# Optimization experiments

Measured on AMD Instinct MI355X. Metric: run time of the kernel, lower is better.

The kernel has to match this reference:

```python
import jax, jax.numpy as jnp
import numpy as np

B, T_ENC, T_DEC, E = 16, 512, 128, 512
H = 1024


def setup_inputs() -> dict:
    key = jax.random.key(0)
    ks = jax.random.split(key, 16)
    def rn(k, shape, s=0.02):
        return jax.random.normal(k, shape, jnp.float32) * s
    z = lambda *s: jnp.zeros(s, jnp.float32)
    return {
        "inputs": jax.random.normal(ks[0], (B, T_ENC, E), jnp.float32),
        "padded_mels": jax.random.normal(ks[1], (B, 80, T_DEC), jnp.float32),
        "W_enc": rn(ks[2], (128, E)),
        "W_q": rn(ks[3], (128, H)),
        "W_loc_conv": rn(ks[4], (32, 1, 31)),
        "b_loc_conv": z(32),
        "W_loc_dense": rn(ks[5], (128, 32)),
        "b_loc_dense": z(128),
        "w_e": rn(ks[6], (1, 128)),
        "b_e": z(1),
        "W_p1": rn(ks[7], (256, 80)),
        "W_p2": rn(ks[8], (256, 256)),
        "W_ih1": rn(ks[9], (4 * H, 256 + E)),
        "W_hh1": rn(ks[10], (4 * H, H)),
        "b_ih1": z(4 * H),
        "b_hh1": z(4 * H),
        "W_ih2": rn(ks[11], (4 * H, H)),
        "W_hh2": rn(ks[12], (4 * H, H)),
        "b_ih2": z(4 * H),
        "b_hh2": z(4 * H),
        "W_proj": rn(ks[13], (80, H + E)),
        "b_proj": z(80),
        "W_stop": rn(ks[14], (1, H + E)),
        "b_stop": z(1),
    }


def _lstm_cell(x, h, c, W_ih, W_hh, b_ih, b_hh):
    g = W_ih @ x + b_ih + W_hh @ h + b_hh
    i, f, gg, o = jnp.split(g, 4)  # torch gate order: i, f, g, o
    c = jax.nn.sigmoid(f) * c + jax.nn.sigmoid(i) * jnp.tanh(gg)
    h = jax.nn.sigmoid(o) * jnp.tanh(c)
    return h, c


def _forward(inputs, padded_mels, W_enc, W_q, W_loc_conv, b_loc_conv,
             W_loc_dense, b_loc_dense, w_e, b_e, W_p1, W_p2,
             W_ih1, W_hh1, b_ih1, b_hh1, W_ih2, W_hh2, b_ih2, b_hh2,
             W_proj, b_proj, W_stop, b_stop):
    proc_enc = inputs @ W_enc.T  # (B, T_enc, 128)
    # prepend zero frame, use frames 0..T_dec-1 as teacher-forced inputs
    prev = jnp.concatenate([jnp.zeros((B, 80, 1), inputs.dtype), padded_mels], axis=-1)[:, :, :T_DEC]
    prev = jnp.transpose(prev, (2, 0, 1))  # (T_dec, B, 80)
    # F.dropout(p=0.5) in source defaults to training=True -> always applied; deterministic masks here
    mk = jax.random.key(42)
    m1 = jax.random.bernoulli(jax.random.fold_in(mk, 0), 0.5, (T_DEC, B, 256)).astype(inputs.dtype) * 2.0
    m2 = jax.random.bernoulli(jax.random.fold_in(mk, 1), 0.5, (T_DEC, B, 256)).astype(inputs.dtype) * 2.0

    def lstm2(x_seq):
        # faithful to source: (B,1,768) fed to batch_first=False nn.LSTM ->
        # sequence runs over the batch dim with batch=1 and zero init state each step
        zv = jnp.zeros((H,), x_seq.dtype)
        def cell(carry, x):
            h1, c1, h2, c2 = carry
            h1, c1 = _lstm_cell(x, h1, c1, W_ih1, W_hh1, b_ih1, b_hh1)
            h2, c2 = _lstm_cell(h1, h2, c2, W_ih2, W_hh2, b_ih2, b_hh2)
            return (h1, c1, h2, c2), h2
        _, hs = jax.lax.scan(cell, (zv, zv, zv, zv), x_seq)
        return hs  # (B, 1024)

    def step(carry, xs):
        cum, ctx = carry  # (B, T_enc), (B, E)
        x, d1, d2 = xs
        p = jax.nn.relu(x @ W_p1.T) * d1
        p = jax.nn.relu(p @ W_p2.T) * d2
        h = lstm2(jnp.concatenate([p, ctx], axis=-1))  # (B, 1024)
        q = h @ W_q.T  # (B, 128)
        loc = jax.lax.conv_general_dilated(
            cum[:, None, :], W_loc_conv, (1,), [(15, 15)],
            dimension_numbers=("NCH", "OIH", "NCH")) + b_loc_conv[None, :, None]  # (B, 32, T_enc)
        loc = jnp.transpose(loc, (0, 2, 1)) @ W_loc_dense.T + b_loc_dense  # (B, T_enc, 128)
        e = jnp.tanh(q[:, None, :] + loc + proc_enc) @ w_e[0] + b_e[0]  # (B, T_enc)
        aw = jax.nn.softmax(e, axis=1)
        new_ctx = jnp.einsum("bt,bte->be", aw, inputs)  # (B, E)
        do = jnp.concatenate([h, new_ctx], axis=-1)  # (B, 1536)
        frame = do @ W_proj.T + b_proj  # (B, 80)
        stop = do @ W_stop[0] + b_stop[0]  # (B,)
        return (cum + aw, new_ctx), (frame, stop)

    carry0 = (jnp.zeros((B, T_ENC), inputs.dtype), jnp.zeros((B, E), inputs.dtype))
    _, (mels, stops) = jax.lax.scan(step, carry0, (prev, m1, m2))
    return jnp.transpose(mels, (1, 0, 2)), jnp.transpose(stops, (1, 0))


def reference(inputs, padded_mels, W_enc, W_q, W_loc_conv, b_loc_conv,
              W_loc_dense, b_loc_dense, w_e, b_e, W_p1, W_p2,
              W_ih1, W_hh1, b_ih1, b_hh1, W_ih2, W_hh2, b_ih2, b_hh2,
              W_proj, b_proj, W_stop, b_stop):
    return _forward(inputs, padded_mels, W_enc, W_q, W_loc_conv, b_loc_conv,
                    W_loc_dense, b_loc_dense, w_e, b_e, W_p1, W_p2,
                    W_ih1, W_hh1, b_ih1, b_hh1, W_ih2, W_hh2, b_ih2, b_hh2,
                    W_proj, b_proj, W_stop, b_stop)
```

## Files before the change

### kernel.cpp

```cpp
#include <hip/hip_runtime.h>
#include <hip/hip_bf16.h>
#include <stdint.h>

#define TD 128
#define NB 16
#define TE 512
#define EE 512
#define HH 1024
#define NM 80
#define PP 256
#define NWG 256
#define NTH 512

#define AGENT __HIP_MEMORY_SCOPE_AGENT

typedef float f32x4 __attribute__((ext_vector_type(4)));

__device__ inline void astoref(float* p, float v) {
  __hip_atomic_store(p, v, __ATOMIC_RELAXED, AGENT);
}
__device__ inline void astored(double* p, double v) {
  __hip_atomic_store(p, v, __ATOMIC_RELAXED, AGENT);
}
__device__ inline f32x4 ntload4(const float* p) {
  f32x4 r;
  asm volatile("global_load_dwordx4 %0, %1, off sc0\n\ts_waitcnt vmcnt(0)"
               : "=&v"(r) : "v"(p) : "memory");
  return r;
}
__device__ inline float ntload1f(const float* p) {
  float r;
  asm volatile("global_load_dword %0, %1, off sc0\n\ts_waitcnt vmcnt(0)"
               : "=&v"(r) : "v"(p) : "memory");
  return r;
}
__device__ inline double ntload1d(const double* p) {
  double r;
  asm volatile("global_load_dwordx2 %0, %1, off sc0\n\ts_waitcnt vmcnt(0)"
               : "=&v"(r) : "v"(p) : "memory");
  return r;
}
__device__ inline double dsig(double x) { return 1.0 / (1.0 + exp(-x)); }

__host__ __device__ inline void threefry2x32(uint32_t k0, uint32_t k1,
                                             uint32_t& x0, uint32_t& x1) {
  uint32_t ks0 = k0, ks1 = k1, ks2 = k0 ^ k1 ^ 0x1BD11BDAu;
  x0 += ks0; x1 += ks1;
#define RND(rot) { x0 += x1; x1 = (x1 << (rot)) | (x1 >> (32 - (rot))); x1 ^= x0; }
  RND(13) RND(15) RND(26) RND(6)
  x0 += ks1; x1 += ks2 + 1u;
  RND(17) RND(29) RND(16) RND(24)
  x0 += ks2; x1 += ks0 + 2u;
  RND(13) RND(15) RND(26) RND(6)
  x0 += ks0; x1 += ks1 + 3u;
  RND(17) RND(29) RND(16) RND(24)
  x0 += ks1; x1 += ks2 + 4u;
  RND(13) RND(15) RND(26) RND(6)
  x0 += ks2; x1 += ks0 + 5u;
#undef RND
}

__device__ inline double mask_val(uint32_t ka, uint32_t kb, uint32_t i) {
  uint32_t x0 = 0u, x1 = i;
  threefry2x32(ka, kb, x0, x1);
  uint32_t bits = x0 ^ x1;
  float u = __uint_as_float((bits >> 9) | 0x3f800000u) - 1.0f;
  return (u < 0.5f) ? 2.0 : 0.0;
}

__global__ void k_proc_enc(const float* __restrict__ inputs,
                           const float* __restrict__ W_enc,
                           float* __restrict__ procTf) {
  int blk = blockIdx.x;
  int b = blk >> 5;
  int t0 = (blk & 31) * 16;
  int d = threadIdx.x;
  __shared__ float in_l[16][EE];
  for (int idx = threadIdx.x; idx < 16 * EE; idx += blockDim.x) {
    int tt = idx >> 9, e = idx & 511;
    in_l[tt][e] = inputs[((size_t)(b * TE + t0 + tt)) * EE + e];
  }
  __syncthreads();
  double acc[16];
#pragma unroll
  for (int tt = 0; tt < 16; ++tt) acc[tt] = 0.0;
  const float* wr = W_enc + (size_t)d * EE;
  for (int e = 0; e < EE; ++e) {
    double w = (double)wr[e];
#pragma unroll
    for (int tt = 0; tt < 16; ++tt) acc[tt] += w * (double)in_l[tt][e];
  }
  for (int tt = 0; tt < 16; ++tt)
    procTf[((size_t)(b * 128 + d)) * TE + t0 + tt] = (float)acc[tt];
}

__global__ void k_p(const float* __restrict__ pm, const float* __restrict__ Wp1,
                    const float* __restrict__ Wp2,
                    uint32_t k1a, uint32_t k1b, uint32_t k2a, uint32_t k2b,
                    float* __restrict__ p_allf) {
  int sb = blockIdx.x;
  int s = sb >> 4, b = sb & 15;
  int tid = threadIdx.x;
  uint32_t mi = (uint32_t)(sb * PP + tid);
  double d1 = mask_val(k1a, k1b, mi);
  double d2 = mask_val(k2a, k2b, mi);
  __shared__ float x_l[NM];
  __shared__ double p1_l[PP];
  if (tid < NM) x_l[tid] = (s == 0) ? 0.f : pm[(b * NM + tid) * TD + (s - 1)];
  __syncthreads();
  double a = 0.0;
  const float* w1 = Wp1 + tid * NM;
  for (int m = 0; m < NM; ++m) a += (double)w1[m] * (double)x_l[m];
  a = fmax(a, 0.0) * d1;
  p1_l[tid] = a;
  __syncthreads();
  double c = 0.0;
  const float* w2 = Wp2 + tid * PP;
  for (int k = 0; k < PP; ++k) c += (double)w2[k] * p1_l[k];
  c = fmax(c, 0.0) * d2;
  p_allf[sb * PP + tid] = (float)c;
}

__global__ void k_init(double* __restrict__ cumg, float* __restrict__ ctxf,
                       float* __restrict__ h1f, float* __restrict__ h2f,
                       uint32_t* __restrict__ barmem) {
  int tid = threadIdx.x;
  for (int i = tid; i < NB * TE; i += 256) cumg[i] = 0.0;
  for (int i = tid; i < NB * EE; i += 256) ctxf[i] = 0.f;
  for (int i = tid; i < 2 * HH; i += 256) { h1f[i] = 0.f; h2f[i] = 0.f; }
  for (int i = tid; i < 8192; i += 256) barmem[i] = 0u;
}

struct SMEM {
  float wldT[4096];
  float wcl[992];
  double bld[128], we[128], blc[32];
  double b1l[16], b2l[16];
  double g1l[16][16];
  double gA[16], gBC[16];
  double c1l[4], c2l[4];
  double be0;
  union U {
    struct { float h1[1024], h2[1024]; } cell;
    struct { float h[1024]; } pq;
    struct { float ctxall[8192]; } g1p;
    struct { double cum[64], q[128], loc[32][33]; } att;
    struct { float aw[512]; double red[16][32]; } ctxp;
    struct { double red[16]; } soft;
    struct { float hb[1536]; double red[16]; } outp;
  } u;
};

__device__ inline void gridbar(uint32_t* barmem, uint32_t& lgen, int wg, int tid) {
  __syncthreads();
  lgen++;
  if (wg == 0) {
    if (tid == 0)
      (void)__hip_atomic_load(&barmem[0], __ATOMIC_ACQUIRE, AGENT);
    if (tid >= 256 && tid < 511) {
      const uint32_t* fl = &barmem[(tid - 255) * 16];
      while (__hip_atomic_load(fl, __ATOMIC_RELAXED, AGENT) < lgen)
        __builtin_amdgcn_s_sleep(1);
    }
    __syncthreads();
    if (tid < 256) {
      asm volatile("s_waitcnt vmcnt(0)" ::: "memory");
      __hip_atomic_store(&barmem[4096 + tid * 16], lgen, __ATOMIC_RELAXED, AGENT);
    }
  } else {
    if (tid == 0) {
      (void)__hip_atomic_load(&barmem[wg * 16], __ATOMIC_ACQUIRE, AGENT);
      __hip_atomic_store(&barmem[wg * 16], lgen, __ATOMIC_RELAXED, AGENT);
      while (__hip_atomic_load(&barmem[4096 + wg * 16], __ATOMIC_RELAXED, AGENT) < lgen)
        __builtin_amdgcn_s_sleep(1);
    }
  }
  __syncthreads();
}

__global__ __launch_bounds__(NTH)
__attribute__((amdgpu_waves_per_eu(2, 2)))
void k_persist(
    const float* __restrict__ inputs,
    const float* __restrict__ W_q,
    const float* __restrict__ W_lc, const float* __restrict__ b_lc,
    const float* __restrict__ W_ld, const float* __restrict__ b_ld,
    const float* __restrict__ w_e, const float* __restrict__ b_e,
    const float* __restrict__ W_ih1, const float* __restrict__ W_hh1,
    const float* __restrict__ b_ih1, const float* __restrict__ b_hh1,
    const float* __restrict__ W_ih2, const float* __restrict__ W_hh2,
    const float* __restrict__ b_ih2, const float* __restrict__ b_hh2,
    const float* __restrict__ W_proj, const float* __restrict__ b_proj,
    const float* __restrict__ W_stop, const float* __restrict__ b_stop,
    const float* __restrict__ p_allf, const float* __restrict__ procTf,
    float* h1f, float* h2f, float* h_allf, float* qf,
    float* ef, float* awf, double* cumg, float* ctxf,
    uint32_t* barmem, float* out) {
  __shared__ SMEM sm;
  const int wg = blockIdx.x, tid = threadIdx.x;
  const int q = tid >> 5, l = tid & 31;
  const int row = (q >> 2) * 1024 + wg * 4 + (q & 3);
  uint32_t lgen = 0;

  for (int i = tid; i < 4096; i += NTH) sm.wldT[(i & 31) * 128 + (i >> 5)] = W_ld[i];
  for (int i = tid; i < 992; i += NTH) sm.wcl[i] = W_lc[i];
  for (int i = tid; i < 128; i += NTH) { sm.bld[i] = (double)b_ld[i]; sm.we[i] = (double)w_e[i]; }
  if (tid < 32) sm.blc[tid] = (double)b_lc[tid];
  if (tid == 0) sm.be0 = (double)b_e[0];
  if (l == 0) {
    sm.b1l[q] = (double)b_ih1[row] + (double)b_hh1[row];
    sm.b2l[q] = (double)b_ih2[row] + (double)b_hh2[row];
  }

  float wA[32], wB[32], wC[32], wD[24];
#pragma unroll
  for (int k = 0; k < 32; ++k) {
    int c = l + 32 * k;
    wA[k] = W_hh1[(size_t)row * 1024 + c];
    wB[k] = W_ih2[(size_t)row * 1024 + c];
    wC[k] = W_hh2[(size_t)row * 1024 + c];
  }
#pragma unroll
  for (int k = 0; k < 24; ++k) wD[k] = W_ih1[(size_t)row * 768 + l + 32 * k];
#pragma unroll
  for (int k = 0; k < 32; ++k) {
    asm volatile("" : "+v"(wA[k]));
    asm volatile("" : "+v"(wB[k]));
    asm volatile("" : "+v"(wC[k]));
  }
#pragma unroll
  for (int k = 0; k < 24; ++k) asm volatile("" : "+v"(wD[k]));
  __syncthreads();

  {
    for (int j = 0; j < 4; ++j) {
      f32x4 v = ntload4(ctxf + (tid + j * NTH) * 4);
      *(f32x4*)&sm.u.g1p.ctxall[(tid + j * NTH) * 4] = v;
    }
    __syncthreads();
    for (int b = 0; b < 16; ++b) {
      double a = 0.0;
#pragma unroll
      for (int k = 0; k < 8; ++k)
        a += (double)wD[k] * (double)p_allf[((size_t)0 * 16 + b) * 256 + l + 32 * k];
#pragma unroll
      for (int k = 8; k < 24; ++k)
        a += (double)wD[k] * (double)sm.u.g1p.ctxall[b * 512 + l + 32 * k - 256];
#pragma unroll
      for (int m = 1; m <= 16; m <<= 1) a += __shfl_xor(a, m);
      if (l == 0) sm.g1l[b][q] = a + sm.b1l[q];
    }
    __syncthreads();
  }
  gridbar(barmem, lgen, wg, tid);

  for (int s = 0; s < TD; ++s) {
    for (int r = 0; r <= 16; ++r) {
      if (r == 0 && tid < 4) { sm.c1l[tid] = 0.0; sm.c2l[tid] = 0.0; }
      if (tid < 256) {
        f32x4 v = ntload4(h1f + (((r & 1) ^ 1)) * 1024 + tid * 4);
        *(f32x4*)&sm.u.cell.h1[tid * 4] = v;
      } else if (r > 0) {
        f32x4 v = ntload4(h2f + (r & 1) * 1024 + (tid - 256) * 4);
        *(f32x4*)&sm.u.cell.h2[(tid - 256) * 4] = v;
      }
      __syncthreads();

      double a0 = 0.0, a1 = 0.0, a2 = 0.0;
#pragma unroll
      for (int k = 0; k < 32; ++k) {
        double h1v = (double)sm.u.cell.h1[l + 32 * k];
        a0 += (double)wA[k] * h1v;
        a1 += (double)wB[k] * h1v;
        a2 += (double)wC[k] * (double)sm.u.cell.h2[l + 32 * k];
      }
#pragma unroll
      for (int m = 1; m <= 16; m <<= 1) {
        a0 += __shfl_xor(a0, m);
        a1 += __shfl_xor(a1, m);
        a2 += __shfl_xor(a2, m);
      }
      if (l == 0) { sm.gA[q] = a0; sm.gBC[q] = a1 + a2; }
      __syncthreads();

      if (r < 16 && tid < 4) {
        int jj = tid;
        double gi = sm.g1l[r][jj]      + sm.gA[jj];
        double gf = sm.g1l[r][4 + jj]  + sm.gA[4 + jj];
        double gg = sm.g1l[r][8 + jj]  + sm.gA[8 + jj];
        double go = sm.g1l[r][12 + jj] + sm.gA[12 + jj];
        double cn = dsig(gf) * sm.c1l[jj] + dsig(gi) * tanh(gg);
        double hn = dsig(go) * tanh(cn);
        sm.c1l[jj] = cn;
        astoref(h1f + (r & 1) * 1024 + wg * 4 + jj, (float)hn);
      }
      if (r > 0 && tid >= 8 && tid < 12) {
        int jj = tid - 8, b = r - 1;
        double gi = sm.gBC[jj]      + sm.b2l[jj];
        double gf = sm.gBC[4 + jj]  + sm.b2l[4 + jj];
        double gg = sm.gBC[8 + jj]  + sm.b2l[8 + jj];
        double go = sm.gBC[12 + jj] + sm.b2l[12 + jj];
        double cn = dsig(gf) * sm.c2l[jj] + dsig(gi) * tanh(gg);
        double hn = dsig(go) * tanh(cn);
        sm.c2l[jj] = cn;
        astoref(h2f + ((b & 1)) * 1024 + wg * 4 + jj, (float)hn);
        astoref(h_allf + (size_t)b * 1024 + wg * 4 + jj, (float)hn);
      }
      gridbar(barmem, lgen, wg, tid);
    }

    {
      int b = wg >> 4;
      if (tid < 256) {
        f32x4 v = ntload4(h_allf + (size_t)b * 1024 + tid * 4);
        *(f32x4*)&sm.u.pq.h[tid * 4] = v;
      }
      __syncthreads();
      int o = tid >> 6, lane = tid & 63;
      int d = (wg & 15) * 8 + o;
      double a = 0.0;
#pragma unroll
      for (int k = 0; k < 16; ++k) {
        int c = lane + 64 * k;
        a += (double)W_q[(size_t)d * 1024 + c] * (double)sm.u.pq.h[c];
      }
#pragma unroll
      for (int m = 1; m <= 32; m <<= 1) a += __shfl_xor(a, m);
      if (lane == 0) astoref(qf + b * 128 + d, (float)a);
    }
    gridbar(barmem, lgen, wg, tid);

    {
      int b = wg >> 4, t0 = (wg & 15) * 32;
      if (tid < 62) {
        int g = t0 - 15 + tid;
        sm.u.att.cum[tid] = (g >= 0 && g < TE) ? ntload1d(cumg + b * TE + g) : 0.0;
      } else if (tid < 190) {
        sm.u.att.q[tid - 62] = (double)ntload1f(qf + b * 128 + (tid - 62));
      }
      __syncthreads();
#pragma unroll
      for (int it = 0; it < 2; ++it) {
        int task = tid + it * NTH;
        int t = task >> 5, ch = task & 31;
        double v = sm.blc[ch];
#pragma unroll
        for (int k = 0; k < 31; ++k) v += (double)sm.wcl[ch * 31 + k] * sm.u.att.cum[t + k];
        sm.u.att.loc[t][ch] = v;
      }
      __syncthreads();
      int t = tid >> 4, part = tid & 15;
      double en = 0.0;
      for (int k = 0; k < 8; ++k) {
        int d = part + 16 * k;
        double sv = sm.u.att.q[d] + sm.bld[d] +
                    (double)procTf[((size_t)(b * 128 + d)) * TE + t0 + t];
#pragma unroll
        for (int c = 0; c < 32; ++c)
          sv += sm.u.att.loc[t][c] * (double)sm.wldT[c * 128 + d];
        en += tanh(sv) * sm.we[d];
      }
#pragma unroll
      for (int m = 1; m <= 8; m <<= 1) en += __shfl_xor(en, m);
      if (part == 0) astoref(ef + b * TE + t0 + t, (float)(en + sm.be0));
    }
    gridbar(barmem, lgen, wg, tid);

    if (wg < 16) {
      int b = wg;
      double e = (double)ntload1f(ef + b * TE + tid);
      double mx = e;
#pragma unroll
      for (int m = 1; m <= 32; m <<= 1) mx = fmax(mx, __shfl_xor(mx, m));
      if ((tid & 63) == 0) sm.u.soft.red[tid >> 6] = mx;
      __syncthreads();
      if (tid == 0) {
        double mm = sm.u.soft.red[0];
        for (int i = 1; i < 8; ++i) mm = fmax(mm, sm.u.soft.red[i]);
        sm.u.soft.red[0] = mm;
      }
      __syncthreads();
      double p = exp(e - sm.u.soft.red[0]);
      __syncthreads();
      double ssum = p;
#pragma unroll
      for (int m = 1; m <= 32; m <<= 1) ssum += __shfl_xor(ssum, m);
      if ((tid & 63) == 0) sm.u.soft.red[tid >> 6] = ssum;
      __syncthreads();
      if (tid == 0) {
        double t_ = 0.0;
        for (int i = 0; i < 8; ++i) t_ += sm.u.soft.red[i];
        sm.u.soft.red[0] = 1.0 / t_;
      }
      __syncthreads();
      double a = p * sm.u.soft.red[0];
      astoref(awf + b * TE + tid, (float)a);
      astored(cumg + b * TE + tid, ntload1d(cumg + b * TE + tid) + a);
    }
    gridbar(barmem, lgen, wg, tid);

    {
      int b = wg >> 4, e0 = (wg & 15) * 32;
      sm.u.ctxp.aw[tid] = ntload1f(awf + b * TE + tid);
      __syncthreads();
      int e = e0 + (tid & 31), tp = tid >> 5;
      double a = 0.0;
      for (int t = tp * 32; t < tp * 32 + 32; ++t)
        a += (double)sm.u.ctxp.aw[t] * (double)inputs[((size_t)(b * TE + t)) * EE + e];
      sm.u.ctxp.red[tp][tid & 31] = a;
      __syncthreads();
      if (tid < 32) {
        double v = 0.0;
        for (int j = 0; j < 16; ++j) v += sm.u.ctxp.red[j][tid];
        astoref(ctxf + b * EE + e0 + tid, (float)v);
      }
    }
    gridbar(barmem, lgen, wg, tid);

    {
      int b = wg & 15, obase = wg >> 4;
      if (tid < 256) {
        f32x4 v = ntload4(h_allf + (size_t)b * 1024 + tid * 4);
        *(f32x4*)&sm.u.outp.hb[tid * 4] = v;
      } else if (tid < 384) {
        f32x4 v = ntload4(ctxf + b * EE + (tid - 256) * 4);
        *(f32x4*)&sm.u.outp.hb[1024 + (tid - 256) * 4] = v;
      }
      __syncthreads();
      for (int j = 0; j < 6; ++j) {
        int o = obase + 16 * j;
        if (o <= NM) {
          const float* wr = (o < NM) ? (W_proj + (size_t)o * 1536) : W_stop;
          double a = 0.0;
#pragma unroll
          for (int kk = 0; kk < 3; ++kk) {
            int k = tid + kk * NTH;
            a += (double)wr[k] * (double)sm.u.outp.hb[k];
          }
#pragma unroll
          for (int m = 1; m <= 32; m <<= 1) a += __shfl_xor(a, m);
          if ((tid & 63) == 0) sm.u.outp.red[tid >> 6] = a;
          __syncthreads();
          if (tid == 0) {
            double v = 0.0;
            for (int i = 0; i < 8; ++i) v += sm.u.outp.red[i];
            v += (o < NM) ? (double)b_proj[o] : (double)b_stop[0];
            if (o < NM) astoref(out + ((size_t)b * TD + s) * NM + o, (float)v);
            else        astoref(out + (size_t)NB * TD * NM + b * TD + s, (float)v);
          }
          __syncthreads();
        }
      }
      __syncthreads();
      if (s < TD - 1) {
        const int ss = s + 1;
        for (int j = 0; j < 4; ++j) {
          f32x4 v = ntload4(ctxf + (tid + j * NTH) * 4);
          *(f32x4*)&sm.u.g1p.ctxall[(tid + j * NTH) * 4] = v;
        }
        __syncthreads();
        for (int b2 = 0; b2 < 16; ++b2) {
          double a = 0.0;
#pragma unroll
          for (int k = 0; k < 8; ++k)
            a += (double)wD[k] * (double)p_allf[((size_t)ss * 16 + b2) * 256 + l + 32 * k];
#pragma unroll
          for (int k = 8; k < 24; ++k)
            a += (double)wD[k] * (double)sm.u.g1p.ctxall[b2 * 512 + l + 32 * k - 256];
#pragma unroll
          for (int m = 1; m <= 16; m <<= 1) a += __shfl_xor(a, m);
          if (l == 0) sm.g1l[b2][q] = a + sm.b1l[q];
        }
        __syncthreads();
        if (tid < 4) astoref(h1f + 1024 + wg * 4 + tid, 0.f);
        else if (tid < 8) astoref(h2f + 1024 + wg * 4 + (tid - 4), 0.f);
      }
    }
    gridbar(barmem, lgen, wg, tid);
  }
}

extern "C" void kernel_launch(void* const* d_in, const int* in_sizes, int n_in,
                              void* d_out, int out_size, void* d_ws, size_t ws_size,
                              hipStream_t stream) {
  const float* inputs = (const float*)d_in[0];
  const float* pmels  = (const float*)d_in[1];
  const float* W_enc  = (const float*)d_in[2];
  const float* W_q    = (const float*)d_in[3];
  const float* W_lc   = (const float*)d_in[4];
  const float* b_lc   = (const float*)d_in[5];
  const float* W_ld   = (const float*)d_in[6];
  const float* b_ld   = (const float*)d_in[7];
  const float* w_e    = (const float*)d_in[8];
  const float* b_e    = (const float*)d_in[9];
  const float* W_p1   = (const float*)d_in[10];
  const float* W_p2   = (const float*)d_in[11];
  const float* W_ih1  = (const float*)d_in[12];
  const float* W_hh1  = (const float*)d_in[13];
  const float* b_ih1  = (const float*)d_in[14];
  const float* b_hh1  = (const float*)d_in[15];
  const float* W_ih2  = (const float*)d_in[16];
  const float* W_hh2  = (const float*)d_in[17];
  const float* b_ih2  = (const float*)d_in[18];
  const float* b_hh2  = (const float*)d_in[19];
  const float* W_proj = (const float*)d_in[20];
  const float* b_proj = (const float*)d_in[21];
  const float* W_stop = (const float*)d_in[22];
  const float* b_stop = (const float*)d_in[23];
  float* out = (float*)d_out;

  float* ws     = (float*)d_ws;
  float* p_allf = ws;
  float* procTf = p_allf + 524288;
  float* h1f    = procTf + 1048576;
  float* h2f    = h1f + 2048;
  float* h_allf = h2f + 2048;
  float* qf     = h_allf + 16384;
  float* ef     = qf + 2048;
  float* awf    = ef + 8192;
  float* ctxf   = awf + 8192;
  double* cumg  = (double*)(ctxf + 8192);
  uint32_t* barmem = (uint32_t*)(cumg + 8192);

  uint32_t k1a = 0u, k1b = 0u, k2a = 0u, k2b = 1u;
  threefry2x32(0u, 42u, k1a, k1b);
  threefry2x32(0u, 42u, k2a, k2b);

  k_proc_enc<<<512, 128, 0, stream>>>(inputs, W_enc, procTf);
  k_p<<<TD * NB, 256, 0, stream>>>(pmels, W_p1, W_p2, k1a, k1b, k2a, k2b, p_allf);
  k_init<<<1, 256, 0, stream>>>(cumg, ctxf, h1f, h2f, barmem);

  k_persist<<<NWG, NTH, 0, stream>>>(
      inputs, W_q, W_lc, b_lc, W_ld, b_ld, w_e, b_e,
      W_ih1, W_hh1, b_ih1, b_hh1, W_ih2, W_hh2, b_ih2, b_hh2,
      W_proj, b_proj, W_stop, b_stop,
      p_allf, procTf, h1f, h2f, h_allf, qf, ef, awf, cumg, ctxf,
      barmem, out);

  (void)in_sizes; (void)n_in; (void)out_size; (void)ws_size;
}
```

Baseline: 33.80 ms.

## Merge softmax into context stage and fold input-gate precompute into round zero

```diff
diff --git a/kernel.cpp b/kernel.cpp
--- a/kernel.cpp
+++ b/kernel.cpp
@@ -22,7 +22,7 @@
 __device__ inline void astored(double* p, double v) {
   __hip_atomic_store(p, v, __ATOMIC_RELAXED, AGENT);
 }
-__device__ inline f32x4 ntload4(const float* p) {
+__device__ inline f32x4 ntload4(const void* p) {
   f32x4 r;
   asm volatile("global_load_dwordx4 %0, %1, off sc0\n\ts_waitcnt vmcnt(0)"
                : "=&v"(r) : "v"(p) : "memory");
@@ -145,8 +145,7 @@
     struct { float h[1024]; } pq;
     struct { float ctxall[8192]; } g1p;
     struct { double cum[64], q[128], loc[32][33]; } att;
-    struct { float aw[512]; double red[16][32]; } ctxp;
-    struct { double red[16]; } soft;
+    struct { float aw[512]; double red[16][32]; double red8[16]; } ctxp;
     struct { float hb[1536]; double red[16]; } outp;
   } u;
 };
@@ -155,8 +154,6 @@
   __syncthreads();
   lgen++;
   if (wg == 0) {
-    if (tid == 0)
-      (void)__hip_atomic_load(&barmem[0], __ATOMIC_ACQUIRE, AGENT);
     if (tid >= 256 && tid < 511) {
       const uint32_t* fl = &barmem[(tid - 255) * 16];
       while (__hip_atomic_load(fl, __ATOMIC_RELAXED, AGENT) < lgen)
@@ -169,7 +166,6 @@
     }
   } else {
     if (tid == 0) {
-      (void)__hip_atomic_load(&barmem[wg * 16], __ATOMIC_ACQUIRE, AGENT);
       __hip_atomic_store(&barmem[wg * 16], lgen, __ATOMIC_RELAXED, AGENT);
       while (__hip_atomic_load(&barmem[4096 + wg * 16], __ATOMIC_RELAXED, AGENT) < lgen)
         __builtin_amdgcn_s_sleep(1);
@@ -194,7 +190,7 @@
     const float* __restrict__ W_stop, const float* __restrict__ b_stop,
     const float* __restrict__ p_allf, const float* __restrict__ procTf,
     float* h1f, float* h2f, float* h_allf, float* qf,
-    float* ef, float* awf, double* cumg, float* ctxf,
+    float* ef, double* cumg, float* ctxf,
     uint32_t* barmem, float* out) {
   __shared__ SMEM sm;
   const int wg = blockIdx.x, tid = threadIdx.x;
@@ -232,79 +228,89 @@
   for (int k = 0; k < 24; ++k) asm volatile("" : "+v"(wD[k]));
   __syncthreads();
 
-  {
-    for (int j = 0; j < 4; ++j) {
-      f32x4 v = ntload4(ctxf + (tid + j * NTH) * 4);
-      *(f32x4*)&sm.u.g1p.ctxall[(tid + j * NTH) * 4] = v;
-    }
-    __syncthreads();
-    for (int b = 0; b < 16; ++b) {
-      double a = 0.0;
-#pragma unroll
-      for (int k = 0; k < 8; ++k)
-        a += (double)wD[k] * (double)p_allf[((size_t)0 * 16 + b) * 256 + l + 32 * k];
-#pragma unroll
-      for (int k = 8; k < 24; ++k)
-        a += (double)wD[k] * (double)sm.u.g1p.ctxall[b * 512 + l + 32 * k - 256];
-#pragma unroll
-      for (int m = 1; m <= 16; m <<= 1) a += __shfl_xor(a, m);
-      if (l == 0) sm.g1l[b][q] = a + sm.b1l[q];
-    }
-    __syncthreads();
-  }
-  gridbar(barmem, lgen, wg, tid);
-
   for (int s = 0; s < TD; ++s) {
     for (int r = 0; r <= 16; ++r) {
-      if (r == 0 && tid < 4) { sm.c1l[tid] = 0.0; sm.c2l[tid] = 0.0; }
-      if (tid < 256) {
-        f32x4 v = ntload4(h1f + (((r & 1) ^ 1)) * 1024 + tid * 4);
-        *(f32x4*)&sm.u.cell.h1[tid * 4] = v;
-      } else if (r > 0) {
-        f32x4 v = ntload4(h2f + (r & 1) * 1024 + (tid - 256) * 4);
-        *(f32x4*)&sm.u.cell.h2[(tid - 256) * 4] = v;
-      }
-      __syncthreads();
-
-      double a0 = 0.0, a1 = 0.0, a2 = 0.0;
-#pragma unroll
-      for (int k = 0; k < 32; ++k) {
-        double h1v = (double)sm.u.cell.h1[l + 32 * k];
-        a0 += (double)wA[k] * h1v;
-        a1 += (double)wB[k] * h1v;
-        a2 += (double)wC[k] * (double)sm.u.cell.h2[l + 32 * k];
-      }
-#pragma unroll
-      for (int m = 1; m <= 16; m <<= 1) {
-        a0 += __shfl_xor(a0, m);
-        a1 += __shfl_xor(a1, m);
-        a2 += __shfl_xor(a2, m);
-      }
-      if (l == 0) { sm.gA[q] = a0; sm.gBC[q] = a1 + a2; }
-      __syncthreads();
-
-      if (r < 16 && tid < 4) {
-        int jj = tid;
-        double gi = sm.g1l[r][jj]      + sm.gA[jj];
-        double gf = sm.g1l[r][4 + jj]  + sm.gA[4 + jj];
-        double gg = sm.g1l[r][8 + jj]  + sm.gA[8 + jj];
-        double go = sm.g1l[r][12 + jj] + sm.gA[12 + jj];
-        double cn = dsig(gf) * sm.c1l[jj] + dsig(gi) * tanh(gg);
-        double hn = dsig(go) * tanh(cn);
-        sm.c1l[jj] = cn;
-        astoref(h1f + (r & 1) * 1024 + wg * 4 + jj, (float)hn);
-      }
-      if (r > 0 && tid >= 8 && tid < 12) {
-        int jj = tid - 8, b = r - 1;
-        double gi = sm.gBC[jj]      + sm.b2l[jj];
-        double gf = sm.gBC[4 + jj]  + sm.b2l[4 + jj];
-        double gg = sm.gBC[8 + jj]  + sm.b2l[8 + jj];
-        double go = sm.gBC[12 + jj] + sm.b2l[12 + jj];
-        double cn = dsig(gf) * sm.c2l[jj] + dsig(gi) * tanh(gg);
-        double hn = dsig(go) * tanh(cn);
-        sm.c2l[jj] = cn;
-        astoref(h2f + ((b & 1)) * 1024 + wg * 4 + jj, (float)hn);
-        astoref(h_allf + (size_t)b * 1024 + wg * 4 + jj, (float)hn);
+      if (r == 0) {
+        if (tid < 4) { sm.c1l[tid] = 0.0; sm.c2l[tid] = 0.0; }
+        for (int j = 0; j < 4; ++j) {
+          f32x4 v = ntload4(ctxf + (tid + j * NTH) * 4);
+          *(f32x4*)&sm.u.g1p.ctxall[(tid + j * NTH) * 4] = v;
+        }
+        __syncthreads();
+        for (int b2 = 0; b2 < 16; ++b2) {
+          double a = 0.0;
+#pragma unroll
+          for (int k = 0; k < 8; ++k)
+            a += (double)wD[k] * (double)p_allf[((size_t)s * 16 + b2) * 256 + l + 32 * k];
+#pragma unroll
+          for (int k = 8; k < 24; ++k)
+            a += (double)wD[k] * (double)sm.u.g1p.ctxall[b2 * 512 + l + 32 * k - 256];
+#pragma unroll
+          for (int m = 1; m <= 16; m <<= 1) a += __shfl_xor(a, m);
+          if (l == 0) sm.g1l[b2][q] = a + sm.b1l[q];
+        }
+        __syncthreads();
+        if (tid < 4) {
+          int jj = tid;
+          double gi = sm.g1l[0][jj];
+          double gf = sm.g1l[0][4 + jj];
+          double gg = sm.g1l[0][8 + jj];
+          double go = sm.g1l[0][12 + jj];
+          double cn = dsig(gf) * sm.c1l[jj] + dsig(gi) * tanh(gg);
+          double hn = dsig(go) * tanh(cn);
+          sm.c1l[jj] = cn;
+          astoref(h1f + wg * 4 + jj, (float)hn);
+        }
+      } else {
+        if (tid < 256) {
+          f32x4 v = ntload4(h1f + (((r & 1) ^ 1)) * 1024 + tid * 4);
+          *(f32x4*)&sm.u.cell.h1[tid * 4] = v;
+        } else {
+          f32x4 v = ntload4(h2f + (r & 1) * 1024 + (tid - 256) * 4);
+          *(f32x4*)&sm.u.cell.h2[(tid - 256) * 4] = v;
+        }
+        __syncthreads();
+
+        double a0 = 0.0, a1 = 0.0, a2 = 0.0;
+#pragma unroll
+        for (int k = 0; k < 32; ++k) {
+          double h1v = (double)sm.u.cell.h1[l + 32 * k];
+          a0 += (double)wA[k] * h1v;
+          a1 += (double)wB[k] * h1v;
+          a2 += (double)wC[k] * (double)sm.u.cell.h2[l + 32 * k];
+        }
+#pragma unroll
+        for (int m = 1; m <= 16; m <<= 1) {
+          a0 += __shfl_xor(a0, m);
+          a1 += __shfl_xor(a1, m);
+          a2 += __shfl_xor(a2, m);
+        }
+        if (l == 0) { sm.gA[q] = a0; sm.gBC[q] = a1 + a2; }
+        __syncthreads();
+
+        if (r < 16 && tid < 4) {
+          int jj = tid;
+          double gi = sm.g1l[r][jj]      + sm.gA[jj];
+          double gf = sm.g1l[r][4 + jj]  + sm.gA[4 + jj];
+          double gg = sm.g1l[r][8 + jj]  + sm.gA[8 + jj];
+          double go = sm.g1l[r][12 + jj] + sm.gA[12 + jj];
+          double cn = dsig(gf) * sm.c1l[jj] + dsig(gi) * tanh(gg);
+          double hn = dsig(go) * tanh(cn);
+          sm.c1l[jj] = cn;
+          astoref(h1f + (r & 1) * 1024 + wg * 4 + jj, (float)hn);
+        }
+        if (tid >= 8 && tid < 12) {
+          int jj = tid - 8, b = r - 1;
+          double gi = sm.gBC[jj]      + sm.b2l[jj];
+          double gf = sm.gBC[4 + jj]  + sm.b2l[4 + jj];
+          double gg = sm.gBC[8 + jj]  + sm.b2l[8 + jj];
+          double go = sm.gBC[12 + jj] + sm.b2l[12 + jj];
+          double cn = dsig(gf) * sm.c2l[jj] + dsig(gi) * tanh(gg);
+          double hn = dsig(go) * tanh(cn);
+          sm.c2l[jj] = cn;
+          astoref(h2f + ((b & 1)) * 1024 + wg * 4 + jj, (float)hn);
+          astoref(h_allf + (size_t)b * 1024 + wg * 4 + jj, (float)hn);
+        }
       }
       gridbar(barmem, lgen, wg, tid);
     }
@@ -366,48 +372,48 @@
     }
     gridbar(barmem, lgen, wg, tid);
 
-    if (wg < 16) {
-      int b = wg;
-      double e = (double)ntload1f(ef + b * TE + tid);
+    {
+      int b = wg >> 4, e0 = (wg & 15) * 32;
+      if (tid < 128) {
+        f32x4 v = ntload4(ef + b * TE + tid * 4);
+        *(f32x4*)&sm.u.ctxp.aw[tid * 4] = v;
+      }
+      __syncthreads();
+      double e = (double)sm.u.ctxp.aw[tid];
       double mx = e;
 #pragma unroll
       for (int m = 1; m <= 32; m <<= 1) mx = fmax(mx, __shfl_xor(mx, m));
-      if ((tid & 63) == 0) sm.u.soft.red[tid >> 6] = mx;
+      if ((tid & 63) == 0) sm.u.ctxp.red8[tid >> 6] = mx;
       __syncthreads();
       if (tid == 0) {
-        double mm = sm.u.soft.red[0];
-        for (int i = 1; i < 8; ++i) mm = fmax(mm, sm.u.soft.red[i]);
-        sm.u.soft.red[0] = mm;
-      }
-      __syncthreads();
-      double p = exp(e - sm.u.soft.red[0]);
+        double mm = sm.u.ctxp.red8[0];
+        for (int i = 1; i < 8; ++i) mm = fmax(mm, sm.u.ctxp.red8[i]);
+        sm.u.ctxp.red8[0] = mm;
+      }
+      __syncthreads();
+      double p = exp(e - sm.u.ctxp.red8[0]);
       __syncthreads();
       double ssum = p;
 #pragma unroll
       for (int m = 1; m <= 32; m <<= 1) ssum += __shfl_xor(ssum, m);
-      if ((tid & 63) == 0) sm.u.soft.red[tid >> 6] = ssum;
+      if ((tid & 63) == 0) sm.u.ctxp.red8[tid >> 6] = ssum;
       __syncthreads();
       if (tid == 0) {
         double t_ = 0.0;
-        for (int i = 0; i < 8; ++i) t_ += sm.u.soft.red[i];
-        sm.u.soft.red[0] = 1.0 / t_;
-      }
-      __syncthreads();
-      double a = p * sm.u.soft.red[0];
-      astoref(awf + b * TE + tid, (float)a);
-      astored(cumg + b * TE + tid, ntload1d(cumg + b * TE + tid) + a);
-    }
-    gridbar(barmem, lgen, wg, tid);
-
-    {
-      int b = wg >> 4, e0 = (wg & 15) * 32;
-      sm.u.ctxp.aw[tid] = ntload1f(awf + b * TE + tid);
-      __syncthreads();
-      int e = e0 + (tid & 31), tp = tid >> 5;
-      double a = 0.0;
+        for (int i = 0; i < 8; ++i) t_ += sm.u.ctxp.red8[i];
+        sm.u.ctxp.red8[0] = 1.0 / t_;
+      }
+      __syncthreads();
+      double a = p * sm.u.ctxp.red8[0];
+      if ((wg & 15) == 0)
+        astored(cumg + b * TE + tid, ntload1d(cumg + b * TE + tid) + a);
+      sm.u.ctxp.aw[tid] = (float)a;
+      __syncthreads();
+      int e2 = e0 + (tid & 31), tp = tid >> 5;
+      double acc = 0.0;
       for (int t = tp * 32; t < tp * 32 + 32; ++t)
-        a += (double)sm.u.ctxp.aw[t] * (double)inputs[((size_t)(b * TE + t)) * EE + e];
-      sm.u.ctxp.red[tp][tid & 31] = a;
+        acc += (double)sm.u.ctxp.aw[t] * (double)inputs[((size_t)(b * TE + t)) * EE + e2];
+      sm.u.ctxp.red[tp][tid & 31] = acc;
       __syncthreads();
       if (tid < 32) {
         double v = 0.0;
@@ -451,27 +457,7 @@
           __syncthreads();
         }
       }
-      __syncthreads();
       if (s < TD - 1) {
-        const int ss = s + 1;
-        for (int j = 0; j < 4; ++j) {
-          f32x4 v = ntload4(ctxf + (tid + j * NTH) * 4);
-          *(f32x4*)&sm.u.g1p.ctxall[(tid + j * NTH) * 4] = v;
-        }
-        __syncthreads();
-        for (int b2 = 0; b2 < 16; ++b2) {
-          double a = 0.0;
-#pragma unroll
-          for (int k = 0; k < 8; ++k)
-            a += (double)wD[k] * (double)p_allf[((size_t)ss * 16 + b2) * 256 + l + 32 * k];
-#pragma unroll
-          for (int k = 8; k < 24; ++k)
-            a += (double)wD[k] * (double)sm.u.g1p.ctxall[b2 * 512 + l + 32 * k - 256];
-#pragma unroll
-          for (int m = 1; m <= 16; m <<= 1) a += __shfl_xor(a, m);
-          if (l == 0) sm.g1l[b2][q] = a + sm.b1l[q];
-        }
-        __syncthreads();
         if (tid < 4) astoref(h1f + 1024 + wg * 4 + tid, 0.f);
         else if (tid < 8) astoref(h2f + 1024 + wg * 4 + (tid - 4), 0.f);
       }
@@ -517,8 +503,7 @@
   float* h_allf = h2f + 2048;
   float* qf     = h_allf + 16384;
   float* ef     = qf + 2048;
-  float* awf    = ef + 8192;
-  float* ctxf   = awf + 8192;
+  float* ctxf   = ef + 8192;
   double* cumg  = (double*)(ctxf + 8192);
   uint32_t* barmem = (uint32_t*)(cumg + 8192);
 
@@ -534,7 +519,7 @@
       inputs, W_q, W_lc, b_lc, W_ld, b_ld, w_e, b_e,
       W_ih1, W_hh1, b_ih1, b_hh1, W_ih2, W_hh2, b_ih2, b_hh2,
       W_proj, b_proj, W_stop, b_stop,
-      p_allf, procTf, h1f, h2f, h_allf, qf, ef, awf, cumg, ctxf,
+      p_allf, procTf, h1f, h2f, h_allf, qf, ef, cumg, ctxf,
       barmem, out);
 
   (void)in_sizes; (void)n_in; (void)out_size; (void)ws_size;
```

New measurement: 41.10 ms. 1.22x slower.
